# Optimization experiments

Measured on AMD Instinct MI355X. Metric: run time of the kernel, lower is better.

## Reference

```python
import jax, jax.numpy as jnp
import numpy as np

D_IN = 1024
D_OUT = 1024

def setup_inputs() -> dict:
    key = jax.random.key(0)
    k1, k2 = jax.random.split(key)
    x = jax.random.normal(k1, (4, 2048, D_IN), dtype=jnp.float32)
    # Keras 'uniform' initializer: U(-0.05, 0.05); kernel has 4 slices, only 0..2 used
    kernel = jax.random.uniform(k2, (4, D_IN, D_OUT), dtype=jnp.float32, minval=-0.05, maxval=0.05)
    return {"x": x, "kernel": kernel}

def reference(x, kernel):
    # QKV projections: x [b, s, d] @ kernel[i] [d, e]
    WQ = jnp.einsum('bsd,de->bse', x, kernel[0])
    WK = jnp.einsum('bsd,de->bse', x, kernel[1])
    WV = jnp.einsum('bsd,de->bse', x, kernel[2])
    scale = 1.0 / jnp.sqrt(jnp.asarray(D_OUT, dtype=WQ.dtype))
    QK = jnp.einsum('bqe,bke->bqk', WQ, WK) * scale  # [b, s, s]
    A = jax.nn.softmax(QK, axis=-1)
    return jnp.einsum('bqk,bke->bqe', A, WV)  # [b, s, e]
```

## Files before the change

kernel.cpp:

```cpp
#include <hip/hip_runtime.h>
#include <hip/hip_bf16.h>
#include <cstdio>

typedef __bf16  bf16x8 __attribute__((ext_vector_type(8)));
typedef float   f32x4  __attribute__((ext_vector_type(4)));
typedef unsigned short u16;
typedef u16     u16x8  __attribute__((ext_vector_type(8)));
typedef u16     u16x4  __attribute__((ext_vector_type(4)));


__device__ __forceinline__ void gld_lds16(const void* g, void* l) {
  __builtin_amdgcn_global_load_lds(
      (const __attribute__((address_space(1))) unsigned int*)g,
      (__attribute__((address_space(3))) unsigned int*)l,
      16, 0, 0);
}

__device__ __forceinline__ u16 f2bf(float f) {
  union { float f; unsigned int u; } c{f};
  unsigned int u = c.u;
  u += 0x7fffu + ((u >> 16) & 1u);
  return (u16)(u >> 16);
}

__device__ __forceinline__ float bf2f(u16 h) {
  union { unsigned int u; float f; } c{(unsigned int)h << 16};
  return c.f;
}

enum { EPI_QKV = 0, EPI_QK = 1, EPI_PV = 2 };


__global__ __launch_bounds__(256) void prep_kernel(const float* __restrict__ x,
                                                   u16* __restrict__ xbf,
                                                   const float* __restrict__ w,
                                                   u16* __restrict__ wt,
                                                   float* __restrict__ rs) {
  __shared__ float tile[32][33];
  const int bid = blockIdx.x;
  if (bid < 4096) {
    const int i = (bid * 256 + threadIdx.x) * 8;
    float4 a = *(const float4*)(x + i);
    float4 b = *(const float4*)(x + i + 4);
    u16x8 r;
    r[0] = f2bf(a.x); r[1] = f2bf(a.y); r[2] = f2bf(a.z); r[3] = f2bf(a.w);
    r[4] = f2bf(b.x); r[5] = f2bf(b.y); r[6] = f2bf(b.z); r[7] = f2bf(b.w);
    *(u16x8*)(xbf + i) = r;
  } else if (bid < 7168) {
    const int b2 = bid - 4096;
    const int s = b2 >> 10, r = b2 & 1023;
    const int e0 = (r & 31) * 32, d0 = (r >> 5) * 32;
    const int tx = threadIdx.x & 31, ty = threadIdx.x >> 5;
    const float* in = w + (size_t)s * 1048576;
#pragma unroll
    for (int j = 0; j < 4; ++j)
      tile[ty + j * 8][tx] = in[(size_t)(d0 + ty + j * 8) * 1024 + e0 + tx];
    __syncthreads();
    u16* o = wt + (size_t)s * 1048576;
#pragma unroll
    for (int j = 0; j < 4; ++j)
      o[(size_t)(e0 + ty + j * 8) * 1024 + d0 + tx] = f2bf(tile[tx][ty + j * 8]);
  } else {
    const float4 z = {0.f, 0.f, 0.f, 0.f};
#pragma unroll
    for (int j = 0; j < 8; ++j)
      ((float4*)rs)[threadIdx.x + j * 256] = z;
  }
}


template <int GX, int GY, int GZ>
__device__ __forceinline__ void xcd_swz(int& bx, int& by, int& bz) {
  constexpr int NWG = GX * GY * GZ;
  static_assert(NWG % 8 == 0, "grid must be divisible by 8");
  constexpr int Q8 = NWG / 8;
  int flat = blockIdx.x + GX * (blockIdx.y + GY * blockIdx.z);
  flat = (flat & 7) * Q8 + (flat >> 3);
  bx = flat % GX;
  by = (flat / GX) % GY;
  bz = flat / (GX * GY);
}


__device__ __forceinline__ void stage_half(const u16* __restrict__ g, int ld, int k0,
                                           u16* ldsb, int w, int l) {
  const int srow = l >> 3;
  const int scol = ((l & 7) ^ (srow & 7)) * 8;
#pragma unroll
  for (int q = 0; q < 2; ++q) {
    const int r = w * 16 + q * 8;
    gld_lds16(g + (long)(r + srow) * ld + k0 + scol, (void*)(ldsb + r * 64));
  }
}

template <int EPI, int GX, int GY, int GZ>
__global__ __launch_bounds__(512, 2)
void gemm256_bt(const u16* __restrict__ A, const u16* __restrict__ B,
                void* __restrict__ Cv, int K, int lda, int ldb, int ldc,
                long sA, long sB, long sC,
                float* __restrict__ rowsum, u16* __restrict__ auxK, u16* __restrict__ auxV) {
  __shared__ __align__(16) u16 lds[65536];

  const int t = threadIdx.x;
  const int w = t >> 6, l = t & 63;
  const int wm = w >> 2, wn = w & 3;
  const int lr = l & 15, lq = l >> 4;
  const int rsw = l & 7;
  int bxs, bys, bz;
  xcd_swz<GX, GY, GZ>(bxs, bys, bz);
  const int m0 = bys * 256, n0 = bxs * 256;
  const u16* Ar = A + (long)bz * sA + (long)m0 * lda;
  const u16* Br = B + (long)bz * sB + (long)n0 * ldb;

  u16* curA = lds;
  u16* curB = lds + 16384;
  u16* nxtA = lds + 32768;
  u16* nxtB = lds + 49152;

  const int nt = K >> 6;

  f32x4 acc[8][4] = {};

  stage_half(Ar,             lda, 0, curA,        w, l);
  stage_half(Br,             ldb, 0, curB,        w, l);
  stage_half(Br + 128 * ldb, ldb, 0, curB + 8192, w, l);
  stage_half(Ar + 128 * lda, lda, 0, curA + 8192, w, l);
  asm volatile("s_waitcnt vmcnt(4)" ::: "memory");
  if (nt > 1) {
    stage_half(Ar,             lda, 64, nxtA,        w, l);
    stage_half(Br,             ldb, 64, nxtB,        w, l);
    stage_half(Br + 128 * ldb, ldb, 64, nxtB + 8192, w, l);
    asm volatile("s_waitcnt vmcnt(6)" ::: "memory");
  } else {
    asm volatile("s_waitcnt vmcnt(0)" ::: "memory");
  }
  __builtin_amdgcn_s_barrier();

  for (int tt = 0; tt < nt; ++tt) {
    const int kc = tt << 6;
    bf16x8 a0[4][2], a1[4][2], b0[2][2], b1[2][2];

#pragma unroll
    for (int mi = 0; mi < 4; ++mi)
#pragma unroll
      for (int j = 0; j < 2; ++j)
        a0[mi][j] = *(const bf16x8*)(curA + (wm * 128 + mi * 16 + lr) * 64 +
                                     (((j * 4 + lq) ^ rsw) * 8));
#pragma unroll
    for (int ni = 0; ni < 2; ++ni)
#pragma unroll
      for (int j = 0; j < 2; ++j)
        b0[ni][j] = *(const bf16x8*)(curB + (wn * 64 + ni * 16 + lr) * 64 +
                                     (((j * 4 + lq) ^ rsw) * 8));
    if (tt + 1 < nt)
      stage_half(Ar + 128 * lda, lda, kc + 64, nxtA + 8192, w, l);
    __builtin_amdgcn_s_barrier();
    asm volatile("s_waitcnt lgkmcnt(0)" ::: "memory");
    __builtin_amdgcn_sched_barrier(0);
    __builtin_amdgcn_s_setprio(1);
#pragma unroll
    for (int mi = 0; mi < 4; ++mi)
#pragma unroll
      for (int ni = 0; ni < 2; ++ni)
#pragma unroll
        for (int j = 0; j < 2; ++j)
          acc[mi][ni] = __builtin_amdgcn_mfma_f32_16x16x32_bf16(a0[mi][j], b0[ni][j], acc[mi][ni], 0, 0, 0);
    __builtin_amdgcn_s_setprio(0);
    __builtin_amdgcn_s_barrier();

#pragma unroll
    for (int ni = 0; ni < 2; ++ni)
#pragma unroll
      for (int j = 0; j < 2; ++j)
        b1[ni][j] = *(const bf16x8*)(curB + (wn * 64 + (ni + 2) * 16 + lr) * 64 +
                                     (((j * 4 + lq) ^ rsw) * 8));
    __builtin_amdgcn_s_barrier();
    asm volatile("s_waitcnt lgkmcnt(0)" ::: "memory");
    __builtin_amdgcn_sched_barrier(0);
    __builtin_amdgcn_s_setprio(1);
#pragma unroll
    for (int mi = 0; mi < 4; ++mi)
#pragma unroll
      for (int ni = 0; ni < 2; ++ni)
#pragma unroll
        for (int j = 0; j < 2; ++j)
          acc[mi][ni + 2] = __builtin_amdgcn_mfma_f32_16x16x32_bf16(a0[mi][j], b1[ni][j], acc[mi][ni + 2], 0, 0, 0);
    __builtin_amdgcn_s_setprio(0);
    __builtin_amdgcn_s_barrier();

#pragma unroll
    for (int mi = 0; mi < 4; ++mi)
#pragma unroll
      for (int j = 0; j < 2; ++j)
        a1[mi][j] = *(const bf16x8*)(curA + (wm * 128 + (mi + 4) * 16 + lr) * 64 +
                                     (((j * 4 + lq) ^ rsw) * 8));
    if (tt + 2 < nt)
      stage_half(Br, ldb, kc + 128, curB, w, l);
    __builtin_amdgcn_s_barrier();
    asm volatile("s_waitcnt lgkmcnt(0)" ::: "memory");
    __builtin_amdgcn_sched_barrier(0);
    __builtin_amdgcn_s_setprio(1);
#pragma unroll
    for (int mi = 0; mi < 4; ++mi)
#pragma unroll
      for (int ni = 0; ni < 2; ++ni)
#pragma unroll
        for (int j = 0; j < 2; ++j)
          acc[mi + 4][ni + 2] = __builtin_amdgcn_mfma_f32_16x16x32_bf16(a1[mi][j], b1[ni][j], acc[mi + 4][ni + 2], 0, 0, 0);
    __builtin_amdgcn_s_setprio(0);
    __builtin_amdgcn_s_barrier();

    if (tt + 2 < nt) {
      stage_half(Br + 128 * ldb, ldb, kc + 128, curB + 8192, w, l);
      stage_half(Ar,             lda, kc + 128, curA,        w, l);
    }
    __builtin_amdgcn_s_barrier();
    __builtin_amdgcn_sched_barrier(0);
    __builtin_amdgcn_s_setprio(1);
#pragma unroll
    for (int mi = 0; mi < 4; ++mi)
#pragma unroll
      for (int ni = 0; ni < 2; ++ni)
#pragma unroll
        for (int j = 0; j < 2; ++j)
          acc[mi + 4][ni] = __builtin_amdgcn_mfma_f32_16x16x32_bf16(a1[mi][j], b0[ni][j], acc[mi + 4][ni], 0, 0, 0);
    __builtin_amdgcn_s_setprio(0);
    if (tt + 2 < nt)      asm volatile("s_waitcnt vmcnt(6)" ::: "memory");
    else if (tt + 1 < nt) asm volatile("s_waitcnt vmcnt(0)" ::: "memory");
    __builtin_amdgcn_s_barrier();

    { u16* x_ = curA; curA = nxtA; nxtA = x_; }
    { u16* y_ = curB; curB = nxtB; nxtB = y_; }
  }

  if (EPI == EPI_QK) {
#pragma unroll
    for (int mi = 0; mi < 8; ++mi) {
#pragma unroll
      for (int i = 0; i < 4; ++i) {
        const int row = m0 + wm * 128 + mi * 16 + lq * 4 + i;
        float rs = 0.f;
#pragma unroll
        for (int ni = 0; ni < 4; ++ni) {
          const int col = n0 + wn * 64 + ni * 16 + lr;
          const u16 h = f2bf(__expf(acc[mi][ni][i] * 0.03125f));
          ((u16*)Cv)[(long)bz * sC + (long)row * ldc + col] = h;
          rs += bf2f(h);
        }
        rs += __shfl_xor(rs, 1, 64);
        rs += __shfl_xor(rs, 2, 64);
        rs += __shfl_xor(rs, 4, 64);
        rs += __shfl_xor(rs, 8, 64);
        if (lr == 0) atomicAdd(rowsum + bz * 2048 + row, rs);
      }
    }
    return;
  }

  if (EPI == EPI_QKV && n0 >= 2048) {
    u16* tp = lds;
    const int e0 = n0 - 2048;
    const long bb = m0 >> 11;
    const int kbase = m0 & 2047;
    u16* vt_base = auxV + bb * 2097152;
#pragma unroll
    for (int h = 0; h < 2; ++h) {
      __syncthreads();
      if ((wn >> 1) == h) {
        const int cb = (wn & 1) * 64;
#pragma unroll
        for (int mi = 0; mi < 8; ++mi) {
          const int row0 = wm * 128 + mi * 16 + lq * 4;
#pragma unroll
          for (int ni = 0; ni < 4; ++ni) {
            const int col = cb + ni * 16 + lr;
            u16x4 v4;
#pragma unroll
            for (int i = 0; i < 4; ++i) v4[i] = f2bf(acc[mi][ni][i]);
            *(u16x4*)(tp + col * 264 + row0) = v4;
          }
        }
      }
      __syncthreads();
#pragma unroll
      for (int q = 0; q < 8; ++q) {
        const int chunk = q * 512 + t;
        const int c = chunk >> 5, r0 = (chunk & 31) * 8;
        u16x8 v = *(const u16x8*)(tp + c * 264 + r0);
        *(u16x8*)(vt_base + (long)(e0 + h * 128 + c) * 2048 + kbase + r0) = v;
      }
    }
    return;
  }

  u16* qkv_out = (n0 < 1024) ? (u16*)Cv : auxK;
  const int nl0 = n0 & 1023;
#pragma unroll
  for (int mi = 0; mi < 8; ++mi) {
#pragma unroll
    for (int i = 0; i < 4; ++i) {
      const int row = m0 + wm * 128 + mi * 16 + lq * 4 + i;
#pragma unroll
      for (int ni = 0; ni < 4; ++ni)
        qkv_out[(long)row * 1024 + nl0 + wn * 64 + ni * 16 + lr] = f2bf(acc[mi][ni][i]);
    }
  }
}


template <int EPI, int GX, int GY, int GZ>
__global__ __launch_bounds__(256)
void gemm_bt(const u16* __restrict__ A, const u16* __restrict__ B,
             void* __restrict__ Cv, int K, int lda, int ldb, int ldc,
             long sA, long sB, long sC,
             float* __restrict__ rowsum, u16* __restrict__ auxK, u16* __restrict__ auxV) {
  constexpr int LDS_U16 = (EPI == EPI_QKV) ? (128 * 136) : (128 * 128);
  __shared__ __align__(16) u16 lds[LDS_U16];
  u16* As = lds;
  u16* Bs = lds + 128 * 64;

  const int t = threadIdx.x;
  const int w = t >> 6, l = t & 63;
  int bxs, bys, bz;
  xcd_swz<GX, GY, GZ>(bxs, bys, bz);
  const u16* Ab = A + (long)bz * sA;
  const u16* Bb = B + (long)bz * sB;
  const int m0 = bys * 128, n0 = bxs * 128;
  const int wm = w & 1, wn = w >> 1;
  const int lr = l & 15, lq = l >> 4;
  const int srow = l >> 3;
  const int scol = ((l & 7) ^ ((l >> 3) & 7)) * 8;
  const int rsw = l & 7;

  f32x4 acc[4][4] = {};

  for (int k0 = 0; k0 < K; k0 += 64) {
    __syncthreads();
#pragma unroll
    for (int c = 0; c < 4; ++c) {
      const int rb = (w * 4 + c) * 8;
      gld_lds16(Ab + (long)(m0 + rb + srow) * lda + k0 + scol, (void*)(As + rb * 64));
      gld_lds16(Bb + (long)(n0 + rb + srow) * ldb + k0 + scol, (void*)(Bs + rb * 64));
    }
    __syncthreads();
#pragma unroll
    for (int j = 0; j < 2; ++j) {
      bf16x8 af[4], bfr[4];
#pragma unroll
      for (int i = 0; i < 4; ++i) {
        const int ch = ((j * 4 + lq) ^ rsw) * 8;
        af[i]  = *(const bf16x8*)(As + (wm * 64 + i * 16 + lr) * 64 + ch);
        bfr[i] = *(const bf16x8*)(Bs + (wn * 64 + i * 16 + lr) * 64 + ch);
      }
#pragma unroll
      for (int mi = 0; mi < 4; ++mi)
#pragma unroll
        for (int ni = 0; ni < 4; ++ni)
          acc[mi][ni] = __builtin_amdgcn_mfma_f32_16x16x32_bf16(af[mi], bfr[ni], acc[mi][ni], 0, 0, 0);
    }
  }

  if (EPI == EPI_QKV && n0 >= 2048) {
    u16* tp = lds;
    __syncthreads();
#pragma unroll
    for (int mi = 0; mi < 4; ++mi) {
      const int row0 = wm * 64 + mi * 16 + lq * 4;
#pragma unroll
      for (int ni = 0; ni < 4; ++ni) {
        const int col = wn * 64 + ni * 16 + lr;
        u16x4 v4;
#pragma unroll
        for (int i = 0; i < 4; ++i) v4[i] = f2bf(acc[mi][ni][i]);
        *(u16x4*)(tp + col * 136 + row0) = v4;
      }
    }
    __syncthreads();
    const int e0 = n0 - 2048;
    const long bb = m0 >> 11;
    const int kbase = m0 & 2047;
    u16* vt_base = auxV + bb * 2097152;
#pragma unroll
    for (int q = 0; q < 8; ++q) {
      const int chunk = q * 256 + t;
      const int c = chunk >> 4, r0 = (chunk & 15) * 8;
      u16x8 v = *(const u16x8*)(tp + c * 136 + r0);
      *(u16x8*)(vt_base + (long)(e0 + c) * 2048 + kbase + r0) = v;
    }
    return;
  }

  u16* qkv_out = nullptr;
  int nl0 = 0;
  if (EPI == EPI_QKV) {
    qkv_out = (n0 < 1024) ? (u16*)Cv : auxK;
    nl0 = n0 & 1023;
  }

#pragma unroll
  for (int mi = 0; mi < 4; ++mi) {
#pragma unroll
    for (int i = 0; i < 4; ++i) {
      const int row = m0 + wm * 64 + mi * 16 + lq * 4 + i;
      float inv;
      if (EPI == EPI_PV) inv = 1.0f / rowsum[bz * 2048 + row];
      float rs = 0.f;
#pragma unroll
      for (int ni = 0; ni < 4; ++ni) {
        const float val = acc[mi][ni][i];
        if (EPI == EPI_QKV) {
          const int col_l = nl0 + wn * 64 + ni * 16 + lr;
          qkv_out[(long)row * 1024 + col_l] = f2bf(val);
        } else if (EPI == EPI_QK) {
          const int col = n0 + wn * 64 + ni * 16 + lr;
          const u16 h = f2bf(__expf(val * 0.03125f));
          ((u16*)Cv)[(long)bz * sC + (long)row * ldc + col] = h;
          rs += bf2f(h);
        } else {
          const int col = n0 + wn * 64 + ni * 16 + lr;
          ((float*)Cv)[(long)bz * sC + (long)row * ldc + col] = val * inv;
        }
      }
      if (EPI == EPI_QK) {
        rs += __shfl_xor(rs, 1, 64);
        rs += __shfl_xor(rs, 2, 64);
        rs += __shfl_xor(rs, 4, 64);
        rs += __shfl_xor(rs, 8, 64);
        if (lr == 0) atomicAdd(rowsum + bz * 2048 + row, rs);
      }
    }
  }
}


extern "C" void kernel_launch(void* const* d_in, const int* in_sizes, int n_in,
                              void* d_out, int out_size, void* d_ws, size_t ws_size,
                              hipStream_t stream) {
  (void)in_sizes; (void)n_in; (void)out_size;
  const float* x    = (const float*)d_in[0];
  const float* kern = (const float*)d_in[1];
  float* out = (float*)d_out;
  char* ws = (char*)d_ws;
  const size_t MB = 1024 * 1024;
  u16*   xbf  = (u16*)(ws);
  u16*   WT   = (u16*)(ws + 16 * MB);
  u16*   Qc   = (u16*)(ws + 22 * MB);
  u16*   Kc   = (u16*)(ws + 38 * MB);
  u16*   VT   = (u16*)(ws + 54 * MB);
  u16*   SP   = (u16*)(ws + 70 * MB);
  float* RS   = (float*)(ws + 102 * MB);
  if (ws_size < 102 * MB + 32768)
    fprintf(stderr, "WARNING: ws_size %zu too small\n", ws_size);

  prep_kernel<<<7169, 256, 0, stream>>>(x, xbf, kern, WT, RS);
  gemm256_bt<EPI_QKV, 12, 32, 1><<<dim3(12, 32, 1), 512, 0, stream>>>(
      xbf, WT, Qc, 1024, 1024, 1024, 1024, 0, 0, 0, nullptr, Kc, VT);
  gemm256_bt<EPI_QK, 8, 8, 4><<<dim3(8, 8, 4), 512, 0, stream>>>(
      Qc, Kc, SP, 1024, 1024, 1024, 2048,
      2048L * 1024, 2048L * 1024, 2048L * 2048, RS, nullptr, nullptr);
  gemm_bt<EPI_PV, 8, 16, 4><<<dim3(8, 16, 4), 256, 0, stream>>>(
      SP, VT, out, 2048, 2048, 2048, 1024,
      2048L * 2048, 1024L * 2048, 2048L * 1024, RS, nullptr, nullptr);
}
```

Baseline: 240.0 us.

## Compute V transposed directly via separate Wv·xᵀ GEMM instead of LDS transpose epilogue

The fused QKV GEMM now produces only Q and K. A new gemm_bt launch computes Vᵀ = Wvᵀ·xᵀ directly, so its output is already in the transposed layout the PV GEMM needs, and the LDS transpose epilogue in both GEMM kernels is removed. This drops the extra shared-memory staging and synchronisation, and the QKV kernel's LDS footprint shrinks. The cost is one more kernel launch, and the V GEMM runs on the smaller 128-tile kernel instead of the 256-tile one.

```diff
diff --git a/kernel.cpp b/kernel.cpp
--- a/kernel.cpp
+++ b/kernel.cpp
@@ -28,7 +28,7 @@
   return c.f;
 }
 
-enum { EPI_QKV = 0, EPI_QK = 1, EPI_PV = 2 };
+enum { EPI_QKV = 0, EPI_QK = 1, EPI_PV = 2, EPI_VT = 3 };
 
 
 __global__ __launch_bounds__(256) void prep_kernel(const float* __restrict__ x,
@@ -257,42 +257,6 @@
     return;
   }
 
-  if (EPI == EPI_QKV && n0 >= 2048) {
-    u16* tp = lds;
-    const int e0 = n0 - 2048;
-    const long bb = m0 >> 11;
-    const int kbase = m0 & 2047;
-    u16* vt_base = auxV + bb * 2097152;
-#pragma unroll
-    for (int h = 0; h < 2; ++h) {
-      __syncthreads();
-      if ((wn >> 1) == h) {
-        const int cb = (wn & 1) * 64;
-#pragma unroll
-        for (int mi = 0; mi < 8; ++mi) {
-          const int row0 = wm * 128 + mi * 16 + lq * 4;
-#pragma unroll
-          for (int ni = 0; ni < 4; ++ni) {
-            const int col = cb + ni * 16 + lr;
-            u16x4 v4;
-#pragma unroll
-            for (int i = 0; i < 4; ++i) v4[i] = f2bf(acc[mi][ni][i]);
-            *(u16x4*)(tp + col * 264 + row0) = v4;
-          }
-        }
-      }
-      __syncthreads();
-#pragma unroll
-      for (int q = 0; q < 8; ++q) {
-        const int chunk = q * 512 + t;
-        const int c = chunk >> 5, r0 = (chunk & 31) * 8;
-        u16x8 v = *(const u16x8*)(tp + c * 264 + r0);
-        *(u16x8*)(vt_base + (long)(e0 + h * 128 + c) * 2048 + kbase + r0) = v;
-      }
-    }
-    return;
-  }
-
   u16* qkv_out = (n0 < 1024) ? (u16*)Cv : auxK;
   const int nl0 = n0 & 1023;
 #pragma unroll
@@ -314,8 +278,7 @@
              void* __restrict__ Cv, int K, int lda, int ldb, int ldc,
              long sA, long sB, long sC,
              float* __restrict__ rowsum, u16* __restrict__ auxK, u16* __restrict__ auxV) {
-  constexpr int LDS_U16 = (EPI == EPI_QKV) ? (128 * 136) : (128 * 128);
-  __shared__ __align__(16) u16 lds[LDS_U16];
+  __shared__ __align__(16) u16 lds[128 * 128];
   u16* As = lds;
   u16* Bs = lds + 128 * 64;
 
@@ -360,43 +323,6 @@
     }
   }
 
-  if (EPI == EPI_QKV && n0 >= 2048) {
-    u16* tp = lds;
-    __syncthreads();
-#pragma unroll
-    for (int mi = 0; mi < 4; ++mi) {
-      const int row0 = wm * 64 + mi * 16 + lq * 4;
-#pragma unroll
-      for (int ni = 0; ni < 4; ++ni) {
-        const int col = wn * 64 + ni * 16 + lr;
-        u16x4 v4;
-#pragma unroll
-        for (int i = 0; i < 4; ++i) v4[i] = f2bf(acc[mi][ni][i]);
-        *(u16x4*)(tp + col * 136 + row0) = v4;
-      }
-    }
-    __syncthreads();
-    const int e0 = n0 - 2048;
-    const long bb = m0 >> 11;
-    const int kbase = m0 & 2047;
-    u16* vt_base = auxV + bb * 2097152;
-#pragma unroll
-    for (int q = 0; q < 8; ++q) {
-      const int chunk = q * 256 + t;
-      const int c = chunk >> 4, r0 = (chunk & 15) * 8;
-      u16x8 v = *(const u16x8*)(tp + c * 136 + r0);
-      *(u16x8*)(vt_base + (long)(e0 + c) * 2048 + kbase + r0) = v;
-    }
-    return;
-  }
-
-  u16* qkv_out = nullptr;
-  int nl0 = 0;
-  if (EPI == EPI_QKV) {
-    qkv_out = (n0 < 1024) ? (u16*)Cv : auxK;
-    nl0 = n0 & 1023;
-  }
-
 #pragma unroll
   for (int mi = 0; mi < 4; ++mi) {
 #pragma unroll
@@ -408,16 +334,14 @@
 #pragma unroll
       for (int ni = 0; ni < 4; ++ni) {
         const float val = acc[mi][ni][i];
-        if (EPI == EPI_QKV) {
-          const int col_l = nl0 + wn * 64 + ni * 16 + lr;
-          qkv_out[(long)row * 1024 + col_l] = f2bf(val);
+        const int col = n0 + wn * 64 + ni * 16 + lr;
+        if (EPI == EPI_VT) {
+          auxV[(long)(col >> 11) * 2097152 + (long)row * 2048 + (col & 2047)] = f2bf(val);
         } else if (EPI == EPI_QK) {
-          const int col = n0 + wn * 64 + ni * 16 + lr;
           const u16 h = f2bf(__expf(val * 0.03125f));
           ((u16*)Cv)[(long)bz * sC + (long)row * ldc + col] = h;
           rs += bf2f(h);
         } else {
-          const int col = n0 + wn * 64 + ni * 16 + lr;
           ((float*)Cv)[(long)bz * sC + (long)row * ldc + col] = val * inv;
         }
       }
@@ -453,8 +377,11 @@
     fprintf(stderr, "WARNING: ws_size %zu too small\n", ws_size);
 
   prep_kernel<<<7169, 256, 0, stream>>>(x, xbf, kern, WT, RS);
-  gemm256_bt<EPI_QKV, 12, 32, 1><<<dim3(12, 32, 1), 512, 0, stream>>>(
-      xbf, WT, Qc, 1024, 1024, 1024, 1024, 0, 0, 0, nullptr, Kc, VT);
+  gemm256_bt<EPI_QKV, 8, 32, 1><<<dim3(8, 32, 1), 512, 0, stream>>>(
+      xbf, WT, Qc, 1024, 1024, 1024, 1024, 0, 0, 0, nullptr, Kc, nullptr);
+  gemm_bt<EPI_VT, 64, 8, 1><<<dim3(64, 8, 1), 256, 0, stream>>>(
+      WT + 2 * 1048576, xbf, nullptr, 1024, 1024, 1024, 2048,
+      0, 0, 0, nullptr, nullptr, VT);
   gemm256_bt<EPI_QK, 8, 8, 4><<<dim3(8, 8, 4), 512, 0, stream>>>(
       Qc, Kc, SP, 1024, 1024, 1024, 2048,
       2048L * 1024, 2048L * 1024, 2048L * 2048, RS, nullptr, nullptr);
```

Result: no change. 242.9 us (+1.2%).
